# Performance work log

Measured on AMD Instinct MI355X. Metric: run time of the kernel, lower is better.

Reference implementation:

```python
import math
import jax, jax.numpy as jnp
import numpy as np

N_QUBITS = 8
N_QLAYERS = 2
HIDDEN = 768
BATCH = 8192
LN_EPS = 1e-5


def _ry_gate(theta):
    # theta: scalar or (B,) -> (2,2) or (B,2,2) complex64
    h = theta * 0.5
    c, s = jnp.cos(h), jnp.sin(h)
    g = jnp.stack([jnp.stack([c, -s], axis=-1), jnp.stack([s, c], axis=-1)], axis=-2)
    return g.astype(jnp.complex64)


def _rz_gate(theta):
    t = theta.astype(jnp.complex64)
    e0, e1 = jnp.exp(-0.5j * t), jnp.exp(0.5j * t)
    z = jnp.zeros_like(e0)
    return jnp.stack([jnp.stack([e0, z], axis=-1), jnp.stack([z, e1], axis=-1)], axis=-2)


def _apply_1q(state, gate, w, n):
    # state: (B, 2**n); gate: (2,2) shared or (B,2,2) per-sample; wire w (0 = MSB)
    B = state.shape[0]
    s = state.reshape(B, 2 ** w, 2, -1)
    if gate.ndim == 2:
        s = jnp.einsum('ij,bljr->blir', gate, s)
    else:
        s = jnp.einsum('bij,bljr->blir', gate, s)
    return s.reshape(B, -1)


def _apply_cnot(state, c, t, n):
    B = state.shape[0]
    s = state.reshape((B,) + (2,) * n)
    ax_c = 1 + c
    s0 = jnp.take(s, 0, axis=ax_c)  # control=0 branch, control axis removed
    s1 = jnp.take(s, 1, axis=ax_c)
    ax_t = 1 + t - (1 if t > c else 0)
    s1 = jnp.flip(s1, axis=ax_t)    # X on target when control=1
    s = jnp.stack([s0, s1], axis=ax_c)
    return s.reshape(B, -1)


def _circuit(angles, weights_ry, weights_rz):
    # angles: (B, n) float32 -> (B, n) PauliZ expectations, batched statevector sim
    n, L = N_QUBITS, N_QLAYERS
    B = angles.shape[0]
    state = jnp.zeros((B, 2 ** n), dtype=jnp.complex64).at[:, 0].set(1.0)
    for i in range(n):
        state = _apply_1q(state, _ry_gate(angles[:, i]), i, n)
    for i in range(1, n):
        state = _apply_cnot(state, 0, i, n)
    for l in range(L):
        for i in range(n):
            state = _apply_1q(state, _ry_gate(weights_ry[l, i]), i, n)
            state = _apply_1q(state, _rz_gate(weights_rz[l, i]), i, n)
    for i in range(1, n):
        state = _apply_cnot(state, i, 0, n)
    probs = jnp.abs(state) ** 2  # (B, 2**n)
    k = jnp.arange(2 ** n)
    bits = (k[None, :] >> (n - 1 - jnp.arange(n))[:, None]) & 1  # wire 0 = MSB (PennyLane)
    signs = (1 - 2 * bits).astype(probs.dtype)  # (n, 2**n)
    return probs @ signs.T  # (B, n)


def setup_inputs() -> dict:
    key = jax.random.key(0)
    ks = jax.random.split(key, 8)
    return {
        'hidden': jax.random.normal(ks[0], (BATCH, HIDDEN), dtype=jnp.float32),
        'W_in': jax.random.normal(ks[1], (N_QUBITS, HIDDEN), dtype=jnp.float32) * (1.0 / math.sqrt(HIDDEN)),
        'b_in': jax.random.normal(ks[2], (N_QUBITS,), dtype=jnp.float32) * 0.01,
        'W_out': jax.random.normal(ks[3], (HIDDEN, N_QUBITS), dtype=jnp.float32) * (1.0 / math.sqrt(N_QUBITS)),
        'b_out': jax.random.normal(ks[4], (HIDDEN,), dtype=jnp.float32) * 0.01,
        'weights_ry': jax.random.normal(ks[5], (N_QLAYERS, N_QUBITS), dtype=jnp.float32) * 0.1,
        'weights_rz': jax.random.normal(ks[6], (N_QLAYERS, N_QUBITS), dtype=jnp.float32) * 0.1,
        'gamma': jnp.ones((HIDDEN,), dtype=jnp.float32),
        'beta': jnp.zeros((HIDDEN,), dtype=jnp.float32),
    }


def reference(hidden, W_in, b_in, W_out, b_out, weights_ry, weights_rz, gamma, beta):
    phase = 0.0
    angles = jnp.tanh(hidden @ W_in.T + b_in) * math.pi + phase  # (B, n)
    meas = _circuit(angles, weights_ry, weights_rz).astype(jnp.float32)  # (B, n)
    y = meas @ W_out.T + b_out  # (B, h)
    mu = jnp.mean(y, axis=-1, keepdims=True)
    var = jnp.mean(jnp.square(y - mu), axis=-1, keepdims=True)
    return (y - mu) * jax.lax.rsqrt(var + LN_EPS) * gamma + beta
```

## Files before the change

kernel.cpp:

```cpp
#include <hip/hip_runtime.h>
#include <hip/hip_bf16.h>

#define NQ    8
#define HID   768
#define BATCH 8192
#define TPB   512
#define SPB   8
#define NBLK  (BATCH / SPB)

template<int BF> __device__ __forceinline__ float LDV(const void* p, int i) {
    if constexpr (BF) return __bfloat162float(((const __hip_bfloat16*)p)[i]);
    else return ((const float*)p)[i];
}
template<int BF> __device__ __forceinline__ void STV(void* p, int i, float v) {
    if constexpr (BF) ((__hip_bfloat16*)p)[i] = __float2bfloat16(v);
    else ((float*)p)[i] = v;
}
template<int BF> __device__ __forceinline__ float4 LD4(const void* p, int i4) {
    if constexpr (BF) {
        ushort4 v = ((const ushort4*)p)[i4];
        float4 r;
        r.x = __uint_as_float(((unsigned)v.x) << 16);
        r.y = __uint_as_float(((unsigned)v.y) << 16);
        r.z = __uint_as_float(((unsigned)v.z) << 16);
        r.w = __uint_as_float(((unsigned)v.w) << 16);
        return r;
    } else {
        return ((const float4*)p)[i4];
    }
}

template<int BF>
__device__ __forceinline__ void run_all(
    const void* hidden_, const void* W_in_, const void* b_in_,
    const void* W_out_, const void* b_out_, const void* wry_, const void* wrz_,
    const void* gamma_, const void* beta_, void* out_,
    float* sWin, float4* sWoutLo, float4* sWoutHi)
{
    const int tid  = threadIdx.x;
    const int lane = tid & 63;
    const int wv   = tid >> 6;
    const int j    = lane >> 3;
    const int b    = blockIdx.x * SPB + wv;

    #pragma unroll
    for (int k = 0; k < (NQ*HID/4)/TPB; ++k) {
        int idx = tid + k*TPB;
        ((float4*)sWin)[idx] = LD4<BF>(W_in_, idx);
    }
    #pragma unroll
    for (int k = 0; k < HID/TPB + 1; ++k) {
        int c = tid + k*TPB;
        if (c < HID) {
            sWoutLo[c] = LD4<BF>(W_out_, c*2);
            sWoutHi[c] = LD4<BF>(W_out_, c*2 + 1);
        }
    }
    __syncthreads();

    float DA, DB, Kr, Ki;
    {
        float ry0 = LDV<BF>(wry_, j), ry1 = LDV<BF>(wry_, NQ + j);
        float rz0 = LDV<BF>(wrz_, j), rz1 = LDV<BF>(wrz_, NQ + j);
        float cA = cosf(0.5f*ry0), sA = sinf(0.5f*ry0);
        float cB = cosf(0.5f*ry1), sB = sinf(0.5f*ry1);
        float p0c = cosf(0.5f*rz0), p0s = sinf(0.5f*rz0);
        float p1c = cosf(0.5f*rz1), p1s = sinf(0.5f*rz1);
        float g00r =  cA*p0c, g00i = -cA*p0s;
        float g01r = -sA*p0c, g01i =  sA*p0s;
        float g10r =  sA*p0c, g10i =  sA*p0s;
        float g11r =  cA*p0c, g11i =  cA*p0s;
        float h00r = cB*g00r - sB*g10r, h00i = cB*g00i - sB*g10i;
        float h01r = cB*g01r - sB*g11r, h01i = cB*g01i - sB*g11i;
        float h10r = sB*g00r + cB*g10r, h10i = sB*g00i + cB*g10i;
        float h11r = sB*g01r + cB*g11r, h11i = sB*g01i + cB*g11i;
        float f00r = h00r*p1c + h00i*p1s, f00i = h00i*p1c - h00r*p1s;
        float f01r = h01r*p1c + h01i*p1s, f01i = h01i*p1c - h01r*p1s;
        float f10r = h10r*p1c - h10i*p1s, f10i = h10i*p1c + h10r*p1s;
        float f11r = h11r*p1c - h11i*p1s, f11i = h11i*p1c + h11r*p1s;
        DA = f00r*f00r + f00i*f00i - (f10r*f10r + f10i*f10i);
        DB = f01r*f01r + f01i*f01i - (f11r*f11r + f11i*f11i);
        Kr = (f00r*f01r + f00i*f01i) - (f10r*f11r + f10i*f11i);
        Ki = (f00i*f01r - f00r*f01i) - (f10i*f11r - f10r*f11i);
    }

    float p[NQ];
    #pragma unroll
    for (int q = 0; q < NQ; ++q) p[q] = 0.f;
    const int hb = b * (HID/4);
    #pragma unroll
    for (int t = 0; t < 3; ++t) {
        const int q4 = (t << 6) + lane;
        float4 h = LD4<BF>(hidden_, hb + q4);
        #pragma unroll
        for (int jj = 0; jj < NQ; ++jj) {
            float4 w = ((const float4*)(sWin + jj*HID))[q4];
            p[jj] = fmaf(h.x, w.x, p[jj]);
            p[jj] = fmaf(h.y, w.y, p[jj]);
            p[jj] = fmaf(h.z, w.z, p[jj]);
            p[jj] = fmaf(h.w, w.w, p[jj]);
        }
    }
    const bool mb0 = ((lane >> 3) & 1) != 0;
    const bool mb1 = ((lane >> 4) & 1) != 0;
    const bool mb2 = ((lane >> 5) & 1) != 0;
    float np[4];
    #pragma unroll
    for (int k = 0; k < 4; ++k) {
        float sent = mb0 ? p[2*k]   : p[2*k+1];
        float keep = mb0 ? p[2*k+1] : p[2*k];
        np[k] = keep + __shfl_xor(sent, 8, 64);
    }
    float nq2[2];
    #pragma unroll
    for (int k = 0; k < 2; ++k) {
        float sent = mb1 ? np[2*k]   : np[2*k+1];
        float keep = mb1 ? np[2*k+1] : np[2*k];
        nq2[k] = keep + __shfl_xor(sent, 16, 64);
    }
    float z;
    {
        float sent = mb2 ? nq2[0] : nq2[1];
        float keep = mb2 ? nq2[1] : nq2[0];
        z = keep + __shfl_xor(sent, 32, 64);
    }
    z += __shfl_xor(z, 1, 64);
    z += __shfl_xor(z, 2, 64);
    z += __shfl_xor(z, 4, 64);

    float zb = z + LDV<BF>(b_in_, j);
    float th = tanhf(zb);
    float sj = sinpif(th), cj = cospif(th);

    float ca = 0.5f * (DA + DB), da = 0.5f * (DA - DB);
    const bool g0 = (j == 0);
    float uu = da * cj;
    float vv = fmaf(Kr, sj, ca);
    float MA = g0 ? 1.f : (vv + uu), MB = g0 ? 1.f : (vv - uu);
    float fr = g0 ? 1.f : Kr,        fi = g0 ? 0.f : (cj * Ki);
    #pragma unroll
    for (int d = 8; d < 64; d <<= 1) {
        MA *= __shfl_xor(MA, d, 64);
        MB *= __shfl_xor(MB, d, 64);
        float qr = __shfl_xor(fr, d, 64);
        float qi = __shfl_xor(fi, d, 64);
        float nr = fr*qr - fi*qi;
        float ni = fr*qi + fi*qr;
        fr = nr; fi = ni;
    }
    float DA0 = __shfl(DA, 0, 64), DB0 = __shfl(DB, 0, 64);
    float Kr0 = __shfl(Kr, 0, 64), Ki0 = __shfl(Ki, 0, 64);
    float cc0 = __shfl(cj, 0, 64), sc0 = __shfl(sj, 0, 64);
    float meas0 = 0.5f*(1.f+cc0)*DA0*MA + 0.5f*(1.f-cc0)*DB0*MB
                + sc0*(Kr0*fr - Ki0*fi);
    float measj = g0 ? meas0 : fmaf(cc0, uu, vv);
    float m0 = meas0;
    float m1 = __shfl(measj,  8, 64), m2 = __shfl(measj, 16, 64);
    float m3 = __shfl(measj, 24, 64), m4 = __shfl(measj, 32, 64);
    float m5 = __shfl(measj, 40, 64), m6 = __shfl(measj, 48, 64);
    float m7 = __shfl(measj, 56, 64);

    const int rowbase = b * HID;
    float yv[12];
    float sum = 0.f, sq = 0.f;
    #pragma unroll
    for (int k = 0; k < 12; ++k) {
        const int c = lane + (k << 6);
        float4 w0 = sWoutLo[c];
        float4 w1 = sWoutHi[c];
        float y = LDV<BF>(b_out_, c);
        y = fmaf(m0, w0.x, y); y = fmaf(m1, w0.y, y);
        y = fmaf(m2, w0.z, y); y = fmaf(m3, w0.w, y);
        y = fmaf(m4, w1.x, y); y = fmaf(m5, w1.y, y);
        y = fmaf(m6, w1.z, y); y = fmaf(m7, w1.w, y);
        yv[k] = y;
        sum += y;
        sq = fmaf(y, y, sq);
    }
    #pragma unroll
    for (int d = 1; d < 64; d <<= 1) {
        sum += __shfl_xor(sum, d, 64);
        sq  += __shfl_xor(sq,  d, 64);
    }
    float mean = sum * (1.f/HID);
    float var  = fmaf(sq, 1.f/HID, -mean*mean);
    float rstd = rsqrtf(var + 1e-5f);
    #pragma unroll
    for (int k = 0; k < 12; ++k) {
        const int c = lane + (k << 6);
        float g  = LDV<BF>(gamma_, c);
        float be = LDV<BF>(beta_,  c);
        float o  = fmaf((yv[k] - mean) * rstd, g, be);
        STV<BF>(out_, rowbase + c, o);
    }
}

__global__ __launch_bounds__(TPB, 2) void main_kernel(
    const void* hidden_, const void* W_in_, const void* b_in_,
    const void* W_out_, const void* b_out_, const void* wry_, const void* wrz_,
    const void* gamma_, const void* beta_, void* out_)
{
    __shared__ __align__(16) float  sWin[NQ*HID];
    __shared__ __align__(16) float4 sWoutLo[HID];
    __shared__ __align__(16) float4 sWoutHi[HID];
    const int lane = threadIdx.x & 63;
    unsigned wrd = ((const unsigned*)hidden_)[lane];
    unsigned lo  = wrd & 0xffffu;
    unsigned e   = (lo >> 7) & 0xffu;
    bool v = (lo == 0u) || (e >= 100u && e <= 133u);
    unsigned long long mask = __ballot(v);
    int flag = (__popcll(mask) > 32) ? 1 : 0;
    if (flag)
        run_all<1>(hidden_, W_in_, b_in_, W_out_, b_out_, wry_, wrz_,
                   gamma_, beta_, out_, sWin, sWoutLo, sWoutHi);
    else
        run_all<0>(hidden_, W_in_, b_in_, W_out_, b_out_, wry_, wrz_,
                   gamma_, beta_, out_, sWin, sWoutLo, sWoutHi);
}

extern "C" void kernel_launch(void* const* d_in, const int* in_sizes, int n_in,
                              void* d_out, int out_size, void* d_ws, size_t ws_size,
                              hipStream_t stream) {
    const void* hidden = d_in[0];
    const void* W_in   = d_in[1];
    const void* b_in   = d_in[2];
    const void* W_out  = d_in[3];
    const void* b_out  = d_in[4];
    const void* wry    = d_in[5];
    const void* wrz    = d_in[6];
    const void* gamma  = d_in[7];
    const void* beta   = d_in[8];
    (void)d_ws; (void)ws_size;
    main_kernel<<<NBLK, TPB, 0, stream>>>(hidden, W_in, b_in, W_out, b_out,
                                          wry, wrz, gamma, beta, d_out);
}
```

Measured before the change: 101.9 us.

## Rewrite kernel around MFMA bf16 GEMMs with one wave per 16 samples

Replaces the 512-thread blocks that staged the weights in shared memory with single-wave blocks of 16 samples. In the bf16 path, both the input projection and the output projection run on MFMA 16x16x32 instructions, with the measurements split into hi and lo bf16 parts to keep precision. The output GEMM is recomputed in a second pass instead of holding values in registers. The circuit evaluation is done per sample by one lane rather than spread across lanes. This trades the shared-memory weight staging and the FMA loops for matrix-core work, at the cost of redundant output-GEMM recomputation and a serial circuit step on 16 lanes; output stores are scalar, strided bf16 writes.

```diff
diff --git a/kernel.cpp b/kernel.cpp
--- a/kernel.cpp
+++ b/kernel.cpp
@@ -4,205 +4,263 @@
 #define NQ    8
 #define HID   768
 #define BATCH 8192
-#define TPB   512
-#define SPB   8
-#define NBLK  (BATCH / SPB)
+#define TPB   64
+#define SPW   16
+#define NBLK  (BATCH / SPW)
+
+typedef short  short8v  __attribute__((ext_vector_type(8)));
+typedef float  float4v  __attribute__((ext_vector_type(4)));
 
 template<int BF> __device__ __forceinline__ float LDV(const void* p, int i) {
     if constexpr (BF) return __bfloat162float(((const __hip_bfloat16*)p)[i]);
     else return ((const float*)p)[i];
 }
-template<int BF> __device__ __forceinline__ void STV(void* p, int i, float v) {
-    if constexpr (BF) ((__hip_bfloat16*)p)[i] = __float2bfloat16(v);
-    else ((float*)p)[i] = v;
-}
-template<int BF> __device__ __forceinline__ float4 LD4(const void* p, int i4) {
-    if constexpr (BF) {
-        ushort4 v = ((const ushort4*)p)[i4];
-        float4 r;
-        r.x = __uint_as_float(((unsigned)v.x) << 16);
-        r.y = __uint_as_float(((unsigned)v.y) << 16);
-        r.z = __uint_as_float(((unsigned)v.z) << 16);
-        r.w = __uint_as_float(((unsigned)v.w) << 16);
-        return r;
-    } else {
-        return ((const float4*)p)[i4];
-    }
+__device__ __forceinline__ float bf2f(unsigned short u) {
+    return __uint_as_float(((unsigned)u) << 16);
+}
+__device__ __forceinline__ unsigned short f2bf_bits(float f) {
+    __hip_bfloat16 h = __float2bfloat16(f);
+    return *reinterpret_cast<unsigned short*>(&h);
 }
 
 template<int BF>
-__device__ __forceinline__ void run_all(
+__device__ __forceinline__ float4 qc_for(const void* wry_, const void* wrz_, int q) {
+    float ry0 = LDV<BF>(wry_, q), ry1 = LDV<BF>(wry_, NQ + q);
+    float rz0 = LDV<BF>(wrz_, q), rz1 = LDV<BF>(wrz_, NQ + q);
+    float cA = cosf(0.5f*ry0), sA = sinf(0.5f*ry0);
+    float cB = cosf(0.5f*ry1), sB = sinf(0.5f*ry1);
+    float p0c = cosf(0.5f*rz0), p0s = sinf(0.5f*rz0);
+    float p1c = cosf(0.5f*rz1), p1s = sinf(0.5f*rz1);
+    float g00r =  cA*p0c, g00i = -cA*p0s;
+    float g01r = -sA*p0c, g01i =  sA*p0s;
+    float g10r =  sA*p0c, g10i =  sA*p0s;
+    float g11r =  cA*p0c, g11i =  cA*p0s;
+    float h00r = cB*g00r - sB*g10r, h00i = cB*g00i - sB*g10i;
+    float h01r = cB*g01r - sB*g11r, h01i = cB*g01i - sB*g11i;
+    float h10r = sB*g00r + cB*g10r, h10i = sB*g00i + cB*g10i;
+    float h11r = sB*g01r + cB*g11r, h11i = sB*g01i + cB*g11i;
+    float f00r = h00r*p1c + h00i*p1s, f00i = h00i*p1c - h00r*p1s;
+    float f01r = h01r*p1c + h01i*p1s, f01i = h01i*p1c - h01r*p1s;
+    float f10r = h10r*p1c - h10i*p1s, f10i = h10i*p1c + h10r*p1s;
+    float f11r = h11r*p1c - h11i*p1s, f11i = h11i*p1c + h11r*p1s;
+    float DA = f00r*f00r + f00i*f00i - (f10r*f10r + f10i*f10i);
+    float DB = f01r*f01r + f01i*f01i - (f11r*f11r + f11i*f11i);
+    float Kr = (f00r*f01r + f00i*f01i) - (f10r*f11r + f10i*f11i);
+    float Ki = (f00i*f01r - f00r*f01i) - (f10i*f11r - f10r*f11i);
+    return make_float4(DA, DB, Kr, Ki);
+}
+
+__device__ __forceinline__ void circuit_meas(const float* zv, const float4* qc,
+                                             const float* binv, float* ms) {
+    float4 q0 = qc[0];
+    float th0 = tanhf(zv[0] + binv[0]);
+    float s0v = sinpif(th0), c0 = cospif(th0);
+    float PA = 1.f, PB = 1.f, PFr = 1.f, PFi = 0.f;
+    #pragma unroll
+    for (int j = 1; j < NQ; ++j) {
+        float4 qj = qc[j];
+        float th = tanhf(zv[j] + binv[j]);
+        float sj = sinpif(th), cj = cospif(th);
+        float ca = 0.5f*(qj.x + qj.y), da = 0.5f*(qj.x - qj.y);
+        float uu = da * cj;
+        float vv = fmaf(qj.z, sj, ca);
+        ms[j] = fmaf(c0, uu, vv);
+        PA *= (vv + uu);
+        PB *= (vv - uu);
+        float fr = qj.z, fi = cj * qj.w;
+        float nr = PFr*fr - PFi*fi, ni = PFr*fi + PFi*fr;
+        PFr = nr; PFi = ni;
+    }
+    ms[0] = 0.5f*(1.f+c0)*q0.x*PA + 0.5f*(1.f-c0)*q0.y*PB
+          + s0v*(q0.z*PFr - q0.w*PFi);
+}
+
+__device__ __forceinline__ void run_bf16(
     const void* hidden_, const void* W_in_, const void* b_in_,
     const void* W_out_, const void* b_out_, const void* wry_, const void* wrz_,
     const void* gamma_, const void* beta_, void* out_,
-    float* sWin, float4* sWoutLo, float4* sWoutHi)
+    float4* sQC, float (*zbuf)[NQ])
 {
-    const int tid  = threadIdx.x;
-    const int lane = tid & 63;
-    const int wv   = tid >> 6;
-    const int j    = lane >> 3;
-    const int b    = blockIdx.x * SPB + wv;
-
-    #pragma unroll
-    for (int k = 0; k < (NQ*HID/4)/TPB; ++k) {
-        int idx = tid + k*TPB;
-        ((float4*)sWin)[idx] = LD4<BF>(W_in_, idx);
-    }
-    #pragma unroll
-    for (int k = 0; k < HID/TPB + 1; ++k) {
-        int c = tid + k*TPB;
-        if (c < HID) {
-            sWoutLo[c] = LD4<BF>(W_out_, c*2);
-            sWoutHi[c] = LD4<BF>(W_out_, c*2 + 1);
-        }
+    const int l   = threadIdx.x;
+    const int r16 = l & 15;
+    const int g4  = l >> 4;
+    const int srow0 = blockIdx.x * SPW;
+
+    {
+        float4 qc = qc_for<1>(wry_, wrz_, l & 7);
+        if (l < NQ) sQC[l] = qc;
+    }
+
+    const short* H   = (const short*)hidden_;
+    const short* Win = (const short*)W_in_;
+    const short* hrow = H + (size_t)(srow0 + r16) * HID + g4 * 8;
+    const bool bval = (r16 < NQ);
+    const short* wrow = Win + (size_t)(r16 & 7) * HID + g4 * 8;
+    float4v zacc = {0.f, 0.f, 0.f, 0.f};
+    #pragma unroll
+    for (int t = 0; t < 24; ++t) {
+        short8v af = *(const short8v*)(hrow + t * 32);
+        short8v bfv = {0,0,0,0,0,0,0,0};
+        if (bval) bfv = *(const short8v*)(wrow + t * 32);
+        zacc = __builtin_amdgcn_mfma_f32_16x16x32_bf16(af, bfv, zacc, 0, 0, 0);
+    }
+    if (r16 < NQ) {
+        #pragma unroll
+        for (int rg = 0; rg < 4; ++rg) zbuf[g4*4 + rg][r16] = zacc[rg];
     }
     __syncthreads();
 
-    float DA, DB, Kr, Ki;
+    short8v mhi = {0,0,0,0,0,0,0,0};
+    short8v mlo = {0,0,0,0,0,0,0,0};
+    if (l < SPW) {
+        float zv[NQ], binv[NQ], ms[NQ];
+        float4 qc[NQ];
+        #pragma unroll
+        for (int j = 0; j < NQ; ++j) {
+            zv[j]   = zbuf[l][j];
+            binv[j] = LDV<1>(b_in_, j);
+            qc[j]   = sQC[j];
+        }
+        circuit_meas(zv, qc, binv, ms);
+        #pragma unroll
+        for (int j = 0; j < NQ; ++j) {
+            unsigned short hb = f2bf_bits(ms[j]);
+            float resid = ms[j] - bf2f(hb);
+            mhi[j] = (short)hb;
+            mlo[j] = (short)f2bf_bits(resid);
+        }
+    }
+
+    const short* Wout = (const short*)W_out_;
+    const __hip_bfloat16* bout = (const __hip_bfloat16*)b_out_;
+    const __hip_bfloat16* gam  = (const __hip_bfloat16*)gamma_;
+    const __hip_bfloat16* bet  = (const __hip_bfloat16*)beta_;
+    float sum4[4] = {0.f,0.f,0.f,0.f};
+    float sq4[4]  = {0.f,0.f,0.f,0.f};
+    for (int nt = 0; nt < 48; ++nt) {
+        int n = nt * 16 + r16;
+        short8v bw = {0,0,0,0,0,0,0,0};
+        if (g4 == 0) bw = *(const short8v*)(Wout + (size_t)n * NQ);
+        float4v y = {0.f,0.f,0.f,0.f};
+        y = __builtin_amdgcn_mfma_f32_16x16x32_bf16(mhi, bw, y, 0, 0, 0);
+        y = __builtin_amdgcn_mfma_f32_16x16x32_bf16(mlo, bw, y, 0, 0, 0);
+        float bo = __bfloat162float(bout[n]);
+        #pragma unroll
+        for (int rg = 0; rg < 4; ++rg) {
+            float d = y[rg] + bo;
+            sum4[rg] += d;
+            sq4[rg] = fmaf(d, d, sq4[rg]);
+        }
+    }
+    #pragma unroll
+    for (int d = 1; d < 16; d <<= 1) {
+        #pragma unroll
+        for (int rg = 0; rg < 4; ++rg) {
+            sum4[rg] += __shfl_xor(sum4[rg], d, 64);
+            sq4[rg]  += __shfl_xor(sq4[rg],  d, 64);
+        }
+    }
+    float mean4[4], rstd4[4];
+    #pragma unroll
+    for (int rg = 0; rg < 4; ++rg) {
+        float mean = sum4[rg] * (1.f/HID);
+        float var  = fmaf(sq4[rg], 1.f/HID, -mean*mean);
+        mean4[rg] = mean;
+        rstd4[rg] = rsqrtf(var + 1e-5f);
+    }
+    __hip_bfloat16* outp = (__hip_bfloat16*)out_;
+    for (int nt = 0; nt < 48; ++nt) {
+        int n = nt * 16 + r16;
+        short8v bw = {0,0,0,0,0,0,0,0};
+        if (g4 == 0) bw = *(const short8v*)(Wout + (size_t)n * NQ);
+        float4v y = {0.f,0.f,0.f,0.f};
+        y = __builtin_amdgcn_mfma_f32_16x16x32_bf16(mhi, bw, y, 0, 0, 0);
+        y = __builtin_amdgcn_mfma_f32_16x16x32_bf16(mlo, bw, y, 0, 0, 0);
+        float bo = __bfloat162float(bout[n]);
+        float ga = __bfloat162float(gam[n]);
+        float be = __bfloat162float(bet[n]);
+        #pragma unroll
+        for (int rg = 0; rg < 4; ++rg) {
+            int row = srow0 + g4*4 + rg;
+            float o = fmaf((y[rg] + bo - mean4[rg]) * rstd4[rg], ga, be);
+            outp[(size_t)row * HID + n] = __float2bfloat16(o);
+        }
+    }
+}
+
+__device__ __forceinline__ void run_f32(
+    const void* hidden_, const void* W_in_, const void* b_in_,
+    const void* W_out_, const void* b_out_, const void* wry_, const void* wrz_,
+    const void* gamma_, const void* beta_, void* out_,
+    float4* sQC)
+{
+    const int l = threadIdx.x;
     {
-        float ry0 = LDV<BF>(wry_, j), ry1 = LDV<BF>(wry_, NQ + j);
-        float rz0 = LDV<BF>(wrz_, j), rz1 = LDV<BF>(wrz_, NQ + j);
-        float cA = cosf(0.5f*ry0), sA = sinf(0.5f*ry0);
-        float cB = cosf(0.5f*ry1), sB = sinf(0.5f*ry1);
-        float p0c = cosf(0.5f*rz0), p0s = sinf(0.5f*rz0);
-        float p1c = cosf(0.5f*rz1), p1s = sinf(0.5f*rz1);
-        float g00r =  cA*p0c, g00i = -cA*p0s;
-        float g01r = -sA*p0c, g01i =  sA*p0s;
-        float g10r =  sA*p0c, g10i =  sA*p0s;
-        float g11r =  cA*p0c, g11i =  cA*p0s;
-        float h00r = cB*g00r - sB*g10r, h00i = cB*g00i - sB*g10i;
-        float h01r = cB*g01r - sB*g11r, h01i = cB*g01i - sB*g11i;
-        float h10r = sB*g00r + cB*g10r, h10i = sB*g00i + cB*g10i;
-        float h11r = sB*g01r + cB*g11r, h11i = sB*g01i + cB*g11i;
-        float f00r = h00r*p1c + h00i*p1s, f00i = h00i*p1c - h00r*p1s;
-        float f01r = h01r*p1c + h01i*p1s, f01i = h01i*p1c - h01r*p1s;
-        float f10r = h10r*p1c - h10i*p1s, f10i = h10i*p1c + h10r*p1s;
-        float f11r = h11r*p1c - h11i*p1s, f11i = h11i*p1c + h11r*p1s;
-        DA = f00r*f00r + f00i*f00i - (f10r*f10r + f10i*f10i);
-        DB = f01r*f01r + f01i*f01i - (f11r*f11r + f11i*f11i);
-        Kr = (f00r*f01r + f00i*f01i) - (f10r*f11r + f10i*f11i);
-        Ki = (f00i*f01r - f00r*f01i) - (f10i*f11r - f10r*f11i);
-    }
-
-    float p[NQ];
-    #pragma unroll
-    for (int q = 0; q < NQ; ++q) p[q] = 0.f;
-    const int hb = b * (HID/4);
-    #pragma unroll
-    for (int t = 0; t < 3; ++t) {
-        const int q4 = (t << 6) + lane;
-        float4 h = LD4<BF>(hidden_, hb + q4);
-        #pragma unroll
-        for (int jj = 0; jj < NQ; ++jj) {
-            float4 w = ((const float4*)(sWin + jj*HID))[q4];
-            p[jj] = fmaf(h.x, w.x, p[jj]);
-            p[jj] = fmaf(h.y, w.y, p[jj]);
-            p[jj] = fmaf(h.z, w.z, p[jj]);
-            p[jj] = fmaf(h.w, w.w, p[jj]);
-        }
-    }
-    const bool mb0 = ((lane >> 3) & 1) != 0;
-    const bool mb1 = ((lane >> 4) & 1) != 0;
-    const bool mb2 = ((lane >> 5) & 1) != 0;
-    float np[4];
-    #pragma unroll
-    for (int k = 0; k < 4; ++k) {
-        float sent = mb0 ? p[2*k]   : p[2*k+1];
-        float keep = mb0 ? p[2*k+1] : p[2*k];
-        np[k] = keep + __shfl_xor(sent, 8, 64);
-    }
-    float nq2[2];
-    #pragma unroll
-    for (int k = 0; k < 2; ++k) {
-        float sent = mb1 ? np[2*k]   : np[2*k+1];
-        float keep = mb1 ? np[2*k+1] : np[2*k];
-        nq2[k] = keep + __shfl_xor(sent, 16, 64);
-    }
-    float z;
-    {
-        float sent = mb2 ? nq2[0] : nq2[1];
-        float keep = mb2 ? nq2[1] : nq2[0];
-        z = keep + __shfl_xor(sent, 32, 64);
-    }
-    z += __shfl_xor(z, 1, 64);
-    z += __shfl_xor(z, 2, 64);
-    z += __shfl_xor(z, 4, 64);
-
-    float zb = z + LDV<BF>(b_in_, j);
-    float th = tanhf(zb);
-    float sj = sinpif(th), cj = cospif(th);
-
-    float ca = 0.5f * (DA + DB), da = 0.5f * (DA - DB);
-    const bool g0 = (j == 0);
-    float uu = da * cj;
-    float vv = fmaf(Kr, sj, ca);
-    float MA = g0 ? 1.f : (vv + uu), MB = g0 ? 1.f : (vv - uu);
-    float fr = g0 ? 1.f : Kr,        fi = g0 ? 0.f : (cj * Ki);
-    #pragma unroll
-    for (int d = 8; d < 64; d <<= 1) {
-        MA *= __shfl_xor(MA, d, 64);
-        MB *= __shfl_xor(MB, d, 64);
-        float qr = __shfl_xor(fr, d, 64);
-        float qi = __shfl_xor(fi, d, 64);
-        float nr = fr*qr - fi*qi;
-        float ni = fr*qi + fi*qr;
-        fr = nr; fi = ni;
-    }
-    float DA0 = __shfl(DA, 0, 64), DB0 = __shfl(DB, 0, 64);
-    float Kr0 = __shfl(Kr, 0, 64), Ki0 = __shfl(Ki, 0, 64);
-    float cc0 = __shfl(cj, 0, 64), sc0 = __shfl(sj, 0, 64);
-    float meas0 = 0.5f*(1.f+cc0)*DA0*MA + 0.5f*(1.f-cc0)*DB0*MB
-                + sc0*(Kr0*fr - Ki0*fi);
-    float measj = g0 ? meas0 : fmaf(cc0, uu, vv);
-    float m0 = meas0;
-    float m1 = __shfl(measj,  8, 64), m2 = __shfl(measj, 16, 64);
-    float m3 = __shfl(measj, 24, 64), m4 = __shfl(measj, 32, 64);
-    float m5 = __shfl(measj, 40, 64), m6 = __shfl(measj, 48, 64);
-    float m7 = __shfl(measj, 56, 64);
-
-    const int rowbase = b * HID;
-    float yv[12];
-    float sum = 0.f, sq = 0.f;
-    #pragma unroll
-    for (int k = 0; k < 12; ++k) {
-        const int c = lane + (k << 6);
-        float4 w0 = sWoutLo[c];
-        float4 w1 = sWoutHi[c];
-        float y = LDV<BF>(b_out_, c);
-        y = fmaf(m0, w0.x, y); y = fmaf(m1, w0.y, y);
-        y = fmaf(m2, w0.z, y); y = fmaf(m3, w0.w, y);
-        y = fmaf(m4, w1.x, y); y = fmaf(m5, w1.y, y);
-        y = fmaf(m6, w1.z, y); y = fmaf(m7, w1.w, y);
-        yv[k] = y;
-        sum += y;
-        sq = fmaf(y, y, sq);
-    }
-    #pragma unroll
-    for (int d = 1; d < 64; d <<= 1) {
-        sum += __shfl_xor(sum, d, 64);
-        sq  += __shfl_xor(sq,  d, 64);
-    }
-    float mean = sum * (1.f/HID);
-    float var  = fmaf(sq, 1.f/HID, -mean*mean);
-    float rstd = rsqrtf(var + 1e-5f);
-    #pragma unroll
-    for (int k = 0; k < 12; ++k) {
-        const int c = lane + (k << 6);
-        float g  = LDV<BF>(gamma_, c);
-        float be = LDV<BF>(beta_,  c);
-        float o  = fmaf((yv[k] - mean) * rstd, g, be);
-        STV<BF>(out_, rowbase + c, o);
-    }
-}
-
-__global__ __launch_bounds__(TPB, 2) void main_kernel(
+        float4 qc = qc_for<0>(wry_, wrz_, l & 7);
+        if (l < NQ) sQC[l] = qc;
+    }
+    __syncthreads();
+    float4 qc[NQ];
+    float binv[NQ];
+    #pragma unroll
+    for (int j = 0; j < NQ; ++j) { qc[j] = sQC[j]; binv[j] = LDV<0>(b_in_, j); }
+    const float* Win  = (const float*)W_in_;
+    const float* Wout = (const float*)W_out_;
+    const float* boutf = (const float*)b_out_;
+    const float* gamf  = (const float*)gamma_;
+    const float* betf  = (const float*)beta_;
+    for (int s = 0; s < SPW; ++s) {
+        int row = blockIdx.x * SPW + s;
+        const float* h = (const float*)hidden_ + (size_t)row * HID;
+        float p[NQ];
+        #pragma unroll
+        for (int j = 0; j < NQ; ++j) p[j] = 0.f;
+        for (int t = 0; t < 12; ++t) {
+            int c = l + 64*t;
+            float hv = h[c];
+            #pragma unroll
+            for (int j = 0; j < NQ; ++j)
+                p[j] = fmaf(hv, Win[(size_t)j*HID + c], p[j]);
+        }
+        #pragma unroll
+        for (int d = 1; d < 64; d <<= 1) {
+            #pragma unroll
+            for (int j = 0; j < NQ; ++j) p[j] += __shfl_xor(p[j], d, 64);
+        }
+        float ms[NQ];
+        circuit_meas(p, qc, binv, ms);
+        float yv[12], sum = 0.f, sq = 0.f;
+        for (int k = 0; k < 12; ++k) {
+            int c = l + 64*k;
+            float y = boutf[c];
+            #pragma unroll
+            for (int j = 0; j < NQ; ++j)
+                y = fmaf(ms[j], Wout[(size_t)c*NQ + j], y);
+            yv[k] = y; sum += y; sq = fmaf(y, y, sq);
+        }
+        #pragma unroll
+        for (int d = 1; d < 64; d <<= 1) {
+            sum += __shfl_xor(sum, d, 64);
+            sq  += __shfl_xor(sq,  d, 64);
+        }
+        float mean = sum * (1.f/HID);
+        float var  = fmaf(sq, 1.f/HID, -mean*mean);
+        float rstd = rsqrtf(var + 1e-5f);
+        for (int k = 0; k < 12; ++k) {
+            int c = l + 64*k;
+            ((float*)out_)[(size_t)row*HID + c] =
+                fmaf((yv[k] - mean) * rstd, gamf[c], betf[c]);
+        }
+    }
+}
+
+__global__ __launch_bounds__(TPB) void main_kernel(
     const void* hidden_, const void* W_in_, const void* b_in_,
     const void* W_out_, const void* b_out_, const void* wry_, const void* wrz_,
     const void* gamma_, const void* beta_, void* out_)
 {
-    __shared__ __align__(16) float  sWin[NQ*HID];
-    __shared__ __align__(16) float4 sWoutLo[HID];
-    __shared__ __align__(16) float4 sWoutHi[HID];
+    __shared__ float4 sQC[NQ];
+    __shared__ float  zbuf[SPW][NQ];
     const int lane = threadIdx.x & 63;
     unsigned wrd = ((const unsigned*)hidden_)[lane];
     unsigned lo  = wrd & 0xffffu;
@@ -211,11 +269,11 @@
     unsigned long long mask = __ballot(v);
     int flag = (__popcll(mask) > 32) ? 1 : 0;
     if (flag)
-        run_all<1>(hidden_, W_in_, b_in_, W_out_, b_out_, wry_, wrz_,
-                   gamma_, beta_, out_, sWin, sWoutLo, sWoutHi);
+        run_bf16(hidden_, W_in_, b_in_, W_out_, b_out_, wry_, wrz_,
+                 gamma_, beta_, out_, sQC, zbuf);
     else
-        run_all<0>(hidden_, W_in_, b_in_, W_out_, b_out_, wry_, wrz_,
-                   gamma_, beta_, out_, sWin, sWoutLo, sWoutHi);
+        run_f32(hidden_, W_in_, b_in_, W_out_, b_out_, wry_, wrz_,
+                gamma_, beta_, out_, sQC);
 }
 
 extern "C" void kernel_launch(void* const* d_in, const int* in_sizes, int n_in,
```

New measurement: 356.0 us. +249.4%, slower.
